# Kernel optimization log

Measured on AMD Instinct MI355X. Metric: run time of the kernel, lower is better.

The kernel has to match this reference:

```python
import jax, jax.numpy as jnp
import numpy as np

N_EMBD = 768
N_HEAD = 12
HEAD_DIM = N_EMBD // N_HEAD  # 64


def apply_rotary_emb(x, cos, sin):
    d = x.shape[-1] // 2
    x1, x2 = x[..., :d], x[..., d:]
    y1 = x1 * cos + x2 * sin
    y2 = x1 * -sin + x2 * cos
    return jnp.concatenate([y1, y2], axis=-1)


def rms_norm(x):
    return x * jax.lax.rsqrt(jnp.mean(jnp.square(x), axis=-1, keepdims=True) + 1e-06)


def setup_inputs() -> dict:
    key = jax.random.key(0)
    ks = jax.random.split(key, 7)
    B, T = 2, 2048
    x = jax.random.normal(ks[0], (B, T, N_EMBD), dtype=jnp.float32)
    # cos/sin broadcast over (B, head) axes of [B, T, H, HEAD_DIM//2]
    cos = jax.random.uniform(ks[1], (T, 1, HEAD_DIM // 2), dtype=jnp.float32)
    sin = jax.random.uniform(ks[2], (T, 1, HEAD_DIM // 2), dtype=jnp.float32)
    scale = 1.0 / np.sqrt(N_EMBD)
    wq = jax.random.normal(ks[3], (N_EMBD, N_EMBD), dtype=jnp.float32) * scale
    wk = jax.random.normal(ks[4], (N_EMBD, N_EMBD), dtype=jnp.float32) * scale
    wv = jax.random.normal(ks[5], (N_EMBD, N_EMBD), dtype=jnp.float32) * scale
    wproj = jax.random.normal(ks[6], (N_EMBD, N_EMBD), dtype=jnp.float32) * scale
    return {"x": x, "cos": cos, "sin": sin, "wq": wq, "wk": wk, "wv": wv, "wproj": wproj}


def reference(x, cos, sin, wq, wk, wv, wproj):
    B, T, C = x.shape
    q = (x @ wq).reshape(B, T, N_HEAD, HEAD_DIM)
    k = (x @ wk).reshape(B, T, N_HEAD, HEAD_DIM)
    v = (x @ wv).reshape(B, T, N_HEAD, HEAD_DIM)
    q = rms_norm(apply_rotary_emb(q, cos, sin))
    k = rms_norm(apply_rotary_emb(k, cos, sin))
    # [B, H, T, T] attention scores (non-causal, as in source)
    attn = jnp.einsum('bqhd,bkhd->bhqk', q, k) / jnp.sqrt(jnp.float32(HEAD_DIM))
    attn = jax.nn.softmax(attn, axis=-1)
    y = jnp.einsum('bhqk,bkhd->bqhd', attn, v).reshape(B, T, C)
    return y @ wproj
```

## Files before the change

kernel.cpp:

```cpp
#include <hip/hip_runtime.h>
#include <hip/hip_bf16.h>
#include <stdint.h>

typedef __attribute__((ext_vector_type(8))) __bf16 bf16x8;
typedef __attribute__((ext_vector_type(4))) __bf16 bf16x4;
typedef __attribute__((ext_vector_type(2))) __bf16 bf16x2;
typedef __attribute__((ext_vector_type(4))) float f32x4;
typedef __attribute__((ext_vector_type(16))) float f32x16;
typedef __attribute__((ext_vector_type(8))) unsigned short u16x8;
typedef __attribute__((ext_vector_type(4))) unsigned int u32x4;

#define DEVI __device__ __forceinline__

DEVI void gload16(const void* g, void* l) {
  __builtin_amdgcn_global_load_lds((const __attribute__((address_space(1))) void*)g,
                                   (__attribute__((address_space(3))) void*)l, 16, 0, 0);
}

DEVI uint32_t pack2(float a, float b) {
  bf16x2 t;
  t[0] = (__bf16)a;
  t[1] = (__bf16)b;
  return __builtin_bit_cast(uint32_t, t);
}

DEVI int vswz(int d) { return ((d ^ (d >> 3)) & 15) << 4; }

__global__ __launch_bounds__(256) void cvt_x_k(const float* __restrict__ x,
                                               __bf16* __restrict__ xb, int n4) {
  int i = blockIdx.x * blockDim.x + threadIdx.x;
  int stride = gridDim.x * blockDim.x;
  for (; i < n4; i += stride) {
    float4 v = ((const float4*)x)[i];
    bf16x4 o;
    o[0] = (__bf16)v.x; o[1] = (__bf16)v.y; o[2] = (__bf16)v.z; o[3] = (__bf16)v.w;
    ((bf16x4*)xb)[i] = o;
  }
}

__global__ __launch_bounds__(256) void wtrans_k(const float* __restrict__ wq,
                                                const float* __restrict__ wk,
                                                const float* __restrict__ wv,
                                                const float* __restrict__ wp,
                                                __bf16* __restrict__ WT) {
  __shared__ float tile[32][33];
  const float* W = (blockIdx.z == 0) ? wq : (blockIdx.z == 1) ? wk : (blockIdx.z == 2) ? wv : wp;
  int n0 = blockIdx.x * 32, k0 = blockIdx.y * 32;
  int tx = threadIdx.x, ty = threadIdx.y;
#pragma unroll
  for (int j = 0; j < 4; ++j)
    tile[ty + 8 * j][tx] = W[(size_t)(k0 + ty + 8 * j) * 768 + n0 + tx];
  __syncthreads();
#pragma unroll
  for (int j = 0; j < 4; ++j)
    WT[(size_t)(blockIdx.z * 768 + n0 + ty + 8 * j) * 768 + k0 + tx] =
        (__bf16)tile[tx][ty + 8 * j];
}

template <int EPI, int BN>
__global__ __launch_bounds__(256) void gemm_k(const __bf16* __restrict__ A,
                                              const __bf16* __restrict__ B,
                                              void* __restrict__ Cout,
                                              const float* __restrict__ cosT,
                                              const float* __restrict__ sinT,
                                              int K, int lda, int ldb, int ldc) {
  constexpr int NF = BN / 32;
  __shared__ __align__(16) __bf16 Al[2][128 * 32];
  __shared__ __align__(16) __bf16 Bl[2][BN * 32];
  const int tid = threadIdx.x, lane = tid & 63, w = tid >> 6;
  const int wm = w >> 1, wn = w & 1;
  const int m0 = blockIdx.y * 128, n0 = blockIdx.x * BN;
  const int c = lane & 15, g = lane >> 4;
  f32x4 acc[4][NF] = {};

  auto stage = [&](int k0, int buf) {
#pragma unroll
    for (int i = 0; i < 2; ++i) {
      int e = (i * 256 + tid) * 8;
      int row = e >> 5, col = e & 31;
      gload16(A + (size_t)(m0 + row) * lda + k0 + col, (char*)&Al[buf][0] + 2 * (size_t)e);
    }
#pragma unroll
    for (int i = 0; i < BN / 64; ++i) {
      int e = (i * 256 + tid) * 8;
      int row = e >> 5, col = e & 31;
      gload16(B + (size_t)(n0 + row) * ldb + k0 + col, (char*)&Bl[buf][0] + 2 * (size_t)e);
    }
  };

  stage(0, 0);
  __syncthreads();
  const int NIT = K / 32;
  for (int t = 0; t < NIT; ++t) {
    const int cur = t & 1;
    if (t + 1 < NIT) stage((t + 1) * 32, cur ^ 1);
    bf16x8 af[4], bfr[NF];
#pragma unroll
    for (int q = 0; q < 4; ++q)
      af[q] = *(const bf16x8*)&Al[cur][(wm * 64 + q * 16 + c) * 32 + 8 * g];
#pragma unroll
    for (int q = 0; q < NF; ++q)
      bfr[q] = *(const bf16x8*)&Bl[cur][(wn * (BN / 2) + q * 16 + c) * 32 + 8 * g];
#pragma unroll
    for (int mf = 0; mf < 4; ++mf)
#pragma unroll
      for (int nf = 0; nf < NF; ++nf)
        acc[mf][nf] = __builtin_amdgcn_mfma_f32_16x16x32_bf16(af[mf], bfr[nf],
                                                              acc[mf][nf], 0, 0, 0);
    __syncthreads();
  }

  if (EPI == 1) {
    __bf16* out = (__bf16*)Cout;
    const int colbase = n0 + wn * 64;
    const int plane = colbase / 768;
#pragma unroll
    for (int mf = 0; mf < 4; ++mf) {
#pragma unroll
      for (int r = 0; r < 4; ++r) {
        int row = m0 + wm * 64 + mf * 16 + 4 * g + r;
        float v0 = acc[mf][0][r], v1 = acc[mf][1][r], v2 = acc[mf][2][r], v3 = acc[mf][3][r];
        float y0, y1, y2, y3;
        if (plane < 2) {
          int t = row & 2047;
          float c0 = cosT[t * 32 + c],      s0 = sinT[t * 32 + c];
          float c1 = cosT[t * 32 + 16 + c], s1 = sinT[t * 32 + 16 + c];
          y0 = v0 * c0 + v2 * s0;
          y2 = v2 * c0 - v0 * s0;
          y1 = v1 * c1 + v3 * s1;
          y3 = v3 * c1 - v1 * s1;
          float ss = y0 * y0 + y1 * y1 + y2 * y2 + y3 * y3;
          ss += __shfl_xor(ss, 1); ss += __shfl_xor(ss, 2);
          ss += __shfl_xor(ss, 4); ss += __shfl_xor(ss, 8);
          float rn = rsqrtf(ss * (1.0f / 64.0f) + 1e-6f);
          y0 *= rn; y1 *= rn; y2 *= rn; y3 *= rn;
        } else {
          y0 = v0; y1 = v1; y2 = v2; y3 = v3;
        }
        size_t base = (size_t)row * ldc + colbase + c;
        out[base +  0] = (__bf16)y0;
        out[base + 16] = (__bf16)y1;
        out[base + 32] = (__bf16)y2;
        out[base + 48] = (__bf16)y3;
      }
    }
  } else {
    float* out = (float*)Cout;
#pragma unroll
    for (int mf = 0; mf < 4; ++mf)
#pragma unroll
      for (int nf = 0; nf < NF; ++nf)
#pragma unroll
        for (int r = 0; r < 4; ++r) {
          int row = m0 + wm * 64 + mf * 16 + 4 * g + r;
          out[(size_t)row * ldc + n0 + wn * (BN / 2) + nf * 16 + c] = acc[mf][nf][r];
        }
  }
}

__global__ __launch_bounds__(256, 2) void attn_k(const __bf16* __restrict__ QKV,
                                                 __bf16* __restrict__ Yb) {
  constexpr int TT = 2048;
  constexpr int NT = TT / 128;
  __shared__ __align__(16) char smem[65536];
  const int tid = threadIdx.x, lane = tid & 63, w = tid >> 6;
  const int q5 = lane & 31, h = lane >> 5;
  const int qb = blockIdx.x, bh = blockIdx.y;
  const int b = bh / 12, hd = bh % 12;
  const size_t ldq = 2304;
  const __bf16* Qg = QKV + (size_t)(b * TT) * ldq + hd * 64;
  const __bf16* Kg = QKV + (size_t)(b * TT) * ldq + 768 + hd * 64;
  const __bf16* Vg = QKV + (size_t)(b * TT) * ldq + 1536 + hd * 64;

  const int qrow = qb * 128 + w * 32 + q5;
  bf16x8 aq[4];
#pragma unroll
  for (int t = 0; t < 4; ++t)
    aq[t] = *(const bf16x8*)(Qg + (size_t)qrow * ldq + t * 16 + 8 * h);

  u16x8 vr[4];
  auto stageK = [&](int kv0, int buf) {
#pragma unroll
    for (int p = 0; p < 4; ++p) {
      int cid = p * 256 + tid;
      int row = cid >> 3, s = cid & 7;
      int srccol = 8 * (s ^ (row & 7));
      gload16(Kg + (size_t)(kv0 + row) * ldq + srccol,
              smem + buf * 16384 + row * 128 + 16 * s);
    }
  };
  auto loadV = [&](int kv0) {
#pragma unroll
    for (int p = 0; p < 2; ++p) {
      int u = p * 256 + tid;
      int kp = u >> 3, d0 = (u & 7) * 8;
      const __bf16* src0 = Vg + (size_t)(kv0 + 2 * kp) * ldq + d0;
      vr[2 * p] = *(const u16x8*)src0;
      vr[2 * p + 1] = *(const u16x8*)(src0 + ldq);
    }
  };
  auto writeV = [&](int buf) {
    char* vb = smem + 32768 + buf * 16384;
#pragma unroll
    for (int p = 0; p < 2; ++p) {
      int u = p * 256 + tid;
      int kp = u >> 3, d0 = (u & 7) * 8;
#pragma unroll
      for (int i = 0; i < 8; ++i) {
        int d = d0 + i;
        int byte = (d * 256 + 4 * kp) ^ vswz(d);
        uint32_t pk = (uint32_t)vr[2 * p][i] | ((uint32_t)vr[2 * p + 1][i] << 16);
        *(uint32_t*)(vb + byte) = pk;
      }
    }
  };

  f32x16 Yacc[2] = {};
  float m_run = -__builtin_inff(), l_run = 0.f;

  stageK(0, 0);
  loadV(0);
  writeV(0);
  __syncthreads();

  for (int t = 0; t < NT; ++t) {
    const int cur = t & 1;
    const char* Kb = smem + cur * 16384;
    const char* Vb = smem + 32768 + cur * 16384;
    if (t + 1 < NT) {
      stageK((t + 1) * 128, cur ^ 1);
      loadV((t + 1) * 128);
    }

    float p_[64];
#pragma unroll
    for (int j = 0; j < 4; ++j) {
      f32x16 S = {};
#pragma unroll
      for (int tt = 0; tt < 4; ++tt) {
        int row = j * 32 + q5;
        int chunk = (2 * tt + h) ^ (q5 & 7);
        bf16x8 kf = *(const bf16x8*)(Kb + row * 128 + 16 * chunk);
        S = __builtin_amdgcn_mfma_f32_32x32x16_bf16(kf, aq[tt], S, 0, 0, 0);
      }
#pragma unroll
      for (int r = 0; r < 16; ++r) p_[j * 16 + r] = S[r];
    }

    float m0 = p_[0], m1 = p_[1], m2 = p_[2], m3 = p_[3];
#pragma unroll
    for (int i = 4; i < 64; i += 4) {
      m0 = fmaxf(m0, p_[i]);     m1 = fmaxf(m1, p_[i + 1]);
      m2 = fmaxf(m2, p_[i + 2]); m3 = fmaxf(m3, p_[i + 3]);
    }
    float mx = fmaxf(fmaxf(m0, m1), fmaxf(m2, m3));
    mx = fmaxf(mx, __shfl_xor(mx, 32));
    mx *= 0.125f;
    if (!__all(mx <= m_run + 5.545f)) {
      float mnew = fmaxf(m_run, mx);
      float corr = __expf(m_run - mnew);
      l_run *= corr;
#pragma unroll
      for (int dh = 0; dh < 2; ++dh)
#pragma unroll
        for (int r = 0; r < 16; ++r) Yacc[dh][r] *= corr;
      m_run = mnew;
    }
    float rs0 = 0.f, rs1 = 0.f, rs2 = 0.f, rs3 = 0.f;
#pragma unroll
    for (int i = 0; i < 64; i += 4) {
      float e0 = __expf(fmaf(p_[i], 0.125f, -m_run));
      float e1 = __expf(fmaf(p_[i + 1], 0.125f, -m_run));
      float e2 = __expf(fmaf(p_[i + 2], 0.125f, -m_run));
      float e3 = __expf(fmaf(p_[i + 3], 0.125f, -m_run));
      p_[i] = e0; p_[i + 1] = e1; p_[i + 2] = e2; p_[i + 3] = e3;
      rs0 += e0; rs1 += e1; rs2 += e2; rs3 += e3;
    }
    float rs = (rs0 + rs1) + (rs2 + rs3);
    rs += __shfl_xor(rs, 32);
    l_run += rs;

#pragma unroll
    for (int j = 0; j < 4; ++j) {
#pragma unroll
      for (int s = 0; s < 2; ++s) {
        const float* ps = p_ + j * 16 + s * 8;
        uint32_t pk01 = pack2(ps[0], ps[1]);
        uint32_t pk23 = pack2(ps[2], ps[3]);
        uint32_t pk45 = pack2(ps[4], ps[5]);
        uint32_t pk67 = pack2(ps[6], ps[7]);
        uint32_t fa = (uint32_t)__shfl_xor((int)(h ? pk01 : pk45), 32);
        uint32_t fb = (uint32_t)__shfl_xor((int)(h ? pk23 : pk67), 32);
        u32x4 pw;
        pw[0] = h ? fa : pk01;
        pw[1] = h ? fb : pk23;
        pw[2] = h ? pk45 : fa;
        pw[3] = h ? pk67 : fb;
        bf16x8 pfrag = __builtin_bit_cast(bf16x8, pw);
        int keyb = j * 64 + s * 32 + 16 * h;
#pragma unroll
        for (int dh = 0; dh < 2; ++dh) {
          int d = dh * 32 + q5;
          int byte = (d * 256 + keyb) ^ vswz(d);
          bf16x8 vf = *(const bf16x8*)(Vb + byte);
          Yacc[dh] = __builtin_amdgcn_mfma_f32_32x32x16_bf16(vf, pfrag, Yacc[dh], 0, 0, 0);
        }
      }
    }
    if (t + 1 < NT) writeV(cur ^ 1);
    __syncthreads();
  }

  float rl = __builtin_amdgcn_rcpf(l_run);
  char* yb = smem + w * (32 * 144);
#pragma unroll
  for (int dh = 0; dh < 2; ++dh)
#pragma unroll
    for (int a = 0; a < 4; ++a) {
      bf16x4 pkv;
#pragma unroll
      for (int i = 0; i < 4; ++i) pkv[i] = (__bf16)(Yacc[dh][a * 4 + i] * rl);
      int d0 = a * 8 + 4 * h + 32 * dh;
      *(bf16x4*)(yb + q5 * 144 + d0 * 2) = pkv;
    }
  __bf16* Yrow = Yb + (size_t)(b * TT + qb * 128 + w * 32) * 768 + hd * 64;
#pragma unroll
  for (int k = 0; k < 4; ++k) {
    int chunk = k * 64 + lane;
    int qr = chunk >> 3, sr = chunk & 7;
    bf16x8 vv = *(const bf16x8*)(yb + qr * 144 + sr * 16);
    *(bf16x8*)(Yrow + (size_t)qr * 768 + sr * 8) = vv;
  }
}

extern "C" void kernel_launch(void* const* d_in, const int* in_sizes, int n_in,
                              void* d_out, int out_size, void* d_ws, size_t ws_size,
                              hipStream_t stream) {
  const float* x = (const float*)d_in[0];
  const float* cosT = (const float*)d_in[1];
  const float* sinT = (const float*)d_in[2];
  const float* wq = (const float*)d_in[3];
  const float* wk = (const float*)d_in[4];
  const float* wv = (const float*)d_in[5];
  const float* wp = (const float*)d_in[6];

  char* ws = (char*)d_ws;
  __bf16* xb   = (__bf16*)(ws);
  __bf16* WT   = (__bf16*)(ws + 6291456);
  __bf16* QKVb = (__bf16*)(ws + 11010048);
  __bf16* Yb   = (__bf16*)(ws + 29884416);

  cvt_x_k<<<2048, 256, 0, stream>>>(x, xb, (4096 * 768) / 4);
  wtrans_k<<<dim3(24, 24, 4), dim3(32, 8), 0, stream>>>(wq, wk, wv, wp, WT);
  gemm_k<1, 128><<<dim3(18, 32), 256, 0, stream>>>(xb, WT, (void*)QKVb, cosT, sinT,
                                                   768, 768, 768, 2304);
  attn_k<<<dim3(16, 24), 256, 0, stream>>>(QKVb, Yb);
  gemm_k<0, 64><<<dim3(12, 32), 256, 0, stream>>>(Yb, WT + (size_t)2304 * 768, d_out,
                                                  nullptr, nullptr, 768, 768, 768, 768);
}
```

Before: 181.6 us.

## Deepen GEMM pipeline, remap blocks per XCD, shrink attention tiles

The GEMM moves from double to quad-buffered LDS and prefetches two stages ahead. It uses explicit vmcnt waits with a raw s_barrier instead of a trailing __syncthreads. Both GEMM and attention use 1D grids remapped so neighbouring tiles land on the same XCD, to improve L2 reuse. Attention drops to 128-thread blocks with 64-row query and KV tiles (768 blocks instead of 384), switches to exp2 with a folded log2e scale, and raises the rescale threshold; in exchange it loses per-block K/V reuse and adds more loop iterations.

```diff
diff --git a/kernel.cpp b/kernel.cpp
--- a/kernel.cpp
+++ b/kernel.cpp
@@ -24,7 +24,7 @@
   return __builtin_bit_cast(uint32_t, t);
 }
 
-DEVI int vswz(int d) { return ((d ^ (d >> 3)) & 15) << 4; }
+DEVI int vswz(int d) { return ((d ^ (d >> 3)) & 7) << 4; }
 
 __global__ __launch_bounds__(256) void cvt_x_k(const float* __restrict__ x,
                                                __bf16* __restrict__ xb, int n4) {
@@ -63,13 +63,18 @@
                                               void* __restrict__ Cout,
                                               const float* __restrict__ cosT,
                                               const float* __restrict__ sinT,
-                                              int K, int lda, int ldb, int ldc) {
+                                              int K, int lda, int ldb, int ldc,
+                                              int nwg, int nxb) {
   constexpr int NF = BN / 32;
-  __shared__ __align__(16) __bf16 Al[2][128 * 32];
-  __shared__ __align__(16) __bf16 Bl[2][BN * 32];
+  constexpr int LPT = 2 + BN / 64;
+  __shared__ __align__(16) __bf16 Al[4][128 * 32];
+  __shared__ __align__(16) __bf16 Bl[4][BN * 32];
   const int tid = threadIdx.x, lane = tid & 63, w = tid >> 6;
   const int wm = w >> 1, wn = w & 1;
-  const int m0 = blockIdx.y * 128, n0 = blockIdx.x * BN;
+  const int bid = blockIdx.x;
+  const int o = (bid & 7) * (nwg >> 3) + (bid >> 3);
+  const int bx = o % nxb, by = o / nxb;
+  const int m0 = by * 128, n0 = bx * BN;
   const int c = lane & 15, g = lane >> 4;
   f32x4 acc[4][NF] = {};
 
@@ -88,12 +93,20 @@
     }
   };
 
+  const int NIT = K / 32;
   stage(0, 0);
-  __syncthreads();
-  const int NIT = K / 32;
+  stage(32, 1);
   for (int t = 0; t < NIT; ++t) {
-    const int cur = t & 1;
-    if (t + 1 < NIT) stage((t + 1) * 32, cur ^ 1);
+    if (t + 2 < NIT) {
+      stage((t + 2) * 32, (t + 2) & 3);
+      asm volatile("s_waitcnt vmcnt(%0)" ::"i"(2 * LPT) : "memory");
+    } else if (t + 1 < NIT) {
+      asm volatile("s_waitcnt vmcnt(%0)" ::"i"(LPT) : "memory");
+    } else {
+      asm volatile("s_waitcnt vmcnt(0)" ::: "memory");
+    }
+    __builtin_amdgcn_s_barrier();
+    const int cur = t & 3;
     bf16x8 af[4], bfr[NF];
 #pragma unroll
     for (int q = 0; q < 4; ++q)
@@ -107,7 +120,6 @@
       for (int nf = 0; nf < NF; ++nf)
         acc[mf][nf] = __builtin_amdgcn_mfma_f32_16x16x32_bf16(af[mf], bfr[nf],
                                                               acc[mf][nf], 0, 0, 0);
-    __syncthreads();
   }
 
   if (EPI == 1) {
@@ -158,21 +170,22 @@
   }
 }
 
-__global__ __launch_bounds__(256, 2) void attn_k(const __bf16* __restrict__ QKV,
-                                                 __bf16* __restrict__ Yb) {
-  constexpr int TT = 2048;
-  constexpr int NT = TT / 128;
-  __shared__ __align__(16) char smem[65536];
+__global__ __launch_bounds__(128) void attn_k(const __bf16* __restrict__ QKV,
+                                              __bf16* __restrict__ Yb) {
+  constexpr int TT = 2048, KVB = 64, NT = TT / KVB;
+  __shared__ __align__(16) char smem[32768];
   const int tid = threadIdx.x, lane = tid & 63, w = tid >> 6;
   const int q5 = lane & 31, h = lane >> 5;
-  const int qb = blockIdx.x, bh = blockIdx.y;
+  const int bid = blockIdx.x;
+  const int xcd = bid & 7, idx = bid >> 3;
+  const int bh = xcd * 3 + (idx >> 5), qb = idx & 31;
   const int b = bh / 12, hd = bh % 12;
   const size_t ldq = 2304;
   const __bf16* Qg = QKV + (size_t)(b * TT) * ldq + hd * 64;
   const __bf16* Kg = QKV + (size_t)(b * TT) * ldq + 768 + hd * 64;
   const __bf16* Vg = QKV + (size_t)(b * TT) * ldq + 1536 + hd * 64;
 
-  const int qrow = qb * 128 + w * 32 + q5;
+  const int qrow = qb * 64 + w * 32 + q5;
   bf16x8 aq[4];
 #pragma unroll
   for (int t = 0; t < 4; ++t)
@@ -182,17 +195,17 @@
   auto stageK = [&](int kv0, int buf) {
 #pragma unroll
     for (int p = 0; p < 4; ++p) {
-      int cid = p * 256 + tid;
+      int cid = p * 128 + tid;
       int row = cid >> 3, s = cid & 7;
       int srccol = 8 * (s ^ (row & 7));
       gload16(Kg + (size_t)(kv0 + row) * ldq + srccol,
-              smem + buf * 16384 + row * 128 + 16 * s);
+              smem + buf * 8192 + row * 128 + 16 * s);
     }
   };
   auto loadV = [&](int kv0) {
 #pragma unroll
     for (int p = 0; p < 2; ++p) {
-      int u = p * 256 + tid;
+      int u = p * 128 + tid;
       int kp = u >> 3, d0 = (u & 7) * 8;
       const __bf16* src0 = Vg + (size_t)(kv0 + 2 * kp) * ldq + d0;
       vr[2 * p] = *(const u16x8*)src0;
@@ -200,15 +213,15 @@
     }
   };
   auto writeV = [&](int buf) {
-    char* vb = smem + 32768 + buf * 16384;
+    char* vb = smem + 16384 + buf * 8192;
 #pragma unroll
     for (int p = 0; p < 2; ++p) {
-      int u = p * 256 + tid;
+      int u = p * 128 + tid;
       int kp = u >> 3, d0 = (u & 7) * 8;
 #pragma unroll
       for (int i = 0; i < 8; ++i) {
         int d = d0 + i;
-        int byte = (d * 256 + 4 * kp) ^ vswz(d);
+        int byte = (d * 128 + 4 * kp) ^ vswz(d);
         uint32_t pk = (uint32_t)vr[2 * p][i] | ((uint32_t)vr[2 * p + 1][i] << 16);
         *(uint32_t*)(vb + byte) = pk;
       }
@@ -216,7 +229,8 @@
   };
 
   f32x16 Yacc[2] = {};
-  float m_run = -__builtin_inff(), l_run = 0.f;
+  const float SC = 0.18033688f;
+  float m2 = -__builtin_inff(), l_run = 0.f;
 
   stageK(0, 0);
   loadV(0);
@@ -225,16 +239,16 @@
 
   for (int t = 0; t < NT; ++t) {
     const int cur = t & 1;
-    const char* Kb = smem + cur * 16384;
-    const char* Vb = smem + 32768 + cur * 16384;
+    const char* Kb = smem + cur * 8192;
+    const char* Vb = smem + 16384 + cur * 8192;
     if (t + 1 < NT) {
-      stageK((t + 1) * 128, cur ^ 1);
-      loadV((t + 1) * 128);
-    }
-
-    float p_[64];
-#pragma unroll
-    for (int j = 0; j < 4; ++j) {
+      stageK((t + 1) * KVB, cur ^ 1);
+      loadV((t + 1) * KVB);
+    }
+
+    f32x16 Sv[2];
+#pragma unroll
+    for (int j = 0; j < 2; ++j) {
       f32x16 S = {};
 #pragma unroll
       for (int tt = 0; tt < 4; ++tt) {
@@ -243,37 +257,37 @@
         bf16x8 kf = *(const bf16x8*)(Kb + row * 128 + 16 * chunk);
         S = __builtin_amdgcn_mfma_f32_32x32x16_bf16(kf, aq[tt], S, 0, 0, 0);
       }
-#pragma unroll
-      for (int r = 0; r < 16; ++r) p_[j * 16 + r] = S[r];
-    }
-
-    float m0 = p_[0], m1 = p_[1], m2 = p_[2], m3 = p_[3];
-#pragma unroll
-    for (int i = 4; i < 64; i += 4) {
-      m0 = fmaxf(m0, p_[i]);     m1 = fmaxf(m1, p_[i + 1]);
-      m2 = fmaxf(m2, p_[i + 2]); m3 = fmaxf(m3, p_[i + 3]);
-    }
-    float mx = fmaxf(fmaxf(m0, m1), fmaxf(m2, m3));
+      Sv[j] = S;
+    }
+#define SV(i) Sv[(i) >> 4][(i) & 15]
+
+    float m0 = SV(0), m1 = SV(1), m2c = SV(2), m3 = SV(3);
+#pragma unroll
+    for (int i = 4; i < 32; i += 4) {
+      m0 = fmaxf(m0, SV(i));     m1 = fmaxf(m1, SV(i + 1));
+      m2c = fmaxf(m2c, SV(i + 2)); m3 = fmaxf(m3, SV(i + 3));
+    }
+    float mx = fmaxf(fmaxf(m0, m1), fmaxf(m2c, m3));
     mx = fmaxf(mx, __shfl_xor(mx, 32));
-    mx *= 0.125f;
-    if (!__all(mx <= m_run + 5.545f)) {
-      float mnew = fmaxf(m_run, mx);
-      float corr = __expf(m_run - mnew);
+    mx *= SC;
+    if (!__all(mx <= m2 + 8.0f)) {
+      float mn = fmaxf(m2, mx);
+      float corr = __builtin_exp2f(m2 - mn);
       l_run *= corr;
 #pragma unroll
       for (int dh = 0; dh < 2; ++dh)
 #pragma unroll
         for (int r = 0; r < 16; ++r) Yacc[dh][r] *= corr;
-      m_run = mnew;
+      m2 = mn;
     }
     float rs0 = 0.f, rs1 = 0.f, rs2 = 0.f, rs3 = 0.f;
 #pragma unroll
-    for (int i = 0; i < 64; i += 4) {
-      float e0 = __expf(fmaf(p_[i], 0.125f, -m_run));
-      float e1 = __expf(fmaf(p_[i + 1], 0.125f, -m_run));
-      float e2 = __expf(fmaf(p_[i + 2], 0.125f, -m_run));
-      float e3 = __expf(fmaf(p_[i + 3], 0.125f, -m_run));
-      p_[i] = e0; p_[i + 1] = e1; p_[i + 2] = e2; p_[i + 3] = e3;
+    for (int i = 0; i < 32; i += 4) {
+      float e0 = __builtin_exp2f(fmaf(SV(i), SC, -m2));
+      float e1 = __builtin_exp2f(fmaf(SV(i + 1), SC, -m2));
+      float e2 = __builtin_exp2f(fmaf(SV(i + 2), SC, -m2));
+      float e3 = __builtin_exp2f(fmaf(SV(i + 3), SC, -m2));
+      SV(i) = e0; SV(i + 1) = e1; SV(i + 2) = e2; SV(i + 3) = e3;
       rs0 += e0; rs1 += e1; rs2 += e2; rs3 += e3;
     }
     float rs = (rs0 + rs1) + (rs2 + rs3);
@@ -281,14 +295,14 @@
     l_run += rs;
 
 #pragma unroll
-    for (int j = 0; j < 4; ++j) {
+    for (int j = 0; j < 2; ++j) {
 #pragma unroll
       for (int s = 0; s < 2; ++s) {
-        const float* ps = p_ + j * 16 + s * 8;
-        uint32_t pk01 = pack2(ps[0], ps[1]);
-        uint32_t pk23 = pack2(ps[2], ps[3]);
-        uint32_t pk45 = pack2(ps[4], ps[5]);
-        uint32_t pk67 = pack2(ps[6], ps[7]);
+        int e0 = j * 16 + s * 8;
+        uint32_t pk01 = pack2(SV(e0 + 0), SV(e0 + 1));
+        uint32_t pk23 = pack2(SV(e0 + 2), SV(e0 + 3));
+        uint32_t pk45 = pack2(SV(e0 + 4), SV(e0 + 5));
+        uint32_t pk67 = pack2(SV(e0 + 6), SV(e0 + 7));
         uint32_t fa = (uint32_t)__shfl_xor((int)(h ? pk01 : pk45), 32);
         uint32_t fb = (uint32_t)__shfl_xor((int)(h ? pk23 : pk67), 32);
         u32x4 pw;
@@ -301,12 +315,13 @@
 #pragma unroll
         for (int dh = 0; dh < 2; ++dh) {
           int d = dh * 32 + q5;
-          int byte = (d * 256 + keyb) ^ vswz(d);
+          int byte = (d * 128 + keyb) ^ vswz(d);
           bf16x8 vf = *(const bf16x8*)(Vb + byte);
           Yacc[dh] = __builtin_amdgcn_mfma_f32_32x32x16_bf16(vf, pfrag, Yacc[dh], 0, 0, 0);
         }
       }
     }
+#undef SV
     if (t + 1 < NT) writeV(cur ^ 1);
     __syncthreads();
   }
@@ -323,7 +338,8 @@
       int d0 = a * 8 + 4 * h + 32 * dh;
       *(bf16x4*)(yb + q5 * 144 + d0 * 2) = pkv;
     }
-  __bf16* Yrow = Yb + (size_t)(b * TT + qb * 128 + w * 32) * 768 + hd * 64;
+  __syncthreads();
+  __bf16* Yrow = Yb + (size_t)(b * TT + qb * 64 + w * 32) * 768 + hd * 64;
 #pragma unroll
   for (int k = 0; k < 4; ++k) {
     int chunk = k * 64 + lane;
@@ -352,9 +368,9 @@
 
   cvt_x_k<<<2048, 256, 0, stream>>>(x, xb, (4096 * 768) / 4);
   wtrans_k<<<dim3(24, 24, 4), dim3(32, 8), 0, stream>>>(wq, wk, wv, wp, WT);
-  gemm_k<1, 128><<<dim3(18, 32), 256, 0, stream>>>(xb, WT, (void*)QKVb, cosT, sinT,
-                                                   768, 768, 768, 2304);
-  attn_k<<<dim3(16, 24), 256, 0, stream>>>(QKVb, Yb);
-  gemm_k<0, 64><<<dim3(12, 32), 256, 0, stream>>>(Yb, WT + (size_t)2304 * 768, d_out,
-                                                  nullptr, nullptr, 768, 768, 768, 768);
-}
+  gemm_k<1, 128><<<576, 256, 0, stream>>>(xb, WT, (void*)QKVb, cosT, sinT,
+                                          768, 768, 768, 2304, 576, 18);
+  attn_k<<<768, 128, 0, stream>>>(QKVb, Yb);
+  gemm_k<0, 64><<<384, 256, 0, stream>>>(Yb, WT + (size_t)2304 * 768, d_out,
+                                         nullptr, nullptr, 768, 768, 768, 768, 384, 12);
+}
```

New measurement: 212.1 us. 16.8% more time.
